# Kernel optimization log

Hardware: AMD Instinct MI355X
Metric: run time of the kernel (lower is better)

The kernel has to match this reference:

```python
import jax, jax.numpy as jnp
import numpy as np

B, T, C, H, L, V = 2, 1024, 768, 12, 6, 32000
HS = C // H  # head size 64
EPS = 1e-5


def _ln(x, g, b):
    m = jnp.mean(x, axis=-1, keepdims=True)
    v = jnp.var(x, axis=-1, keepdims=True)
    return (x - m) * jax.lax.rsqrt(v + EPS) * g + b


def setup_inputs() -> dict:
    key = jax.random.key(0)
    ks = iter(jax.random.split(key, 32))
    s = lambda *sh: jax.random.normal(next(ks), sh, jnp.float32) * 0.02
    return {
        "idx": jax.random.randint(next(ks), (B, T), 0, V),
        "tok_emb": s(V, C),
        "pos_emb": s(T, C),
        "Wq": s(L, H, C, HS), "Wk": s(L, H, C, HS), "Wv": s(L, H, C, HS),
        "Wp": s(L, C, C), "bp": jnp.zeros((L, C), jnp.float32),
        "ln1g": jnp.ones((L, C), jnp.float32), "ln1b": jnp.zeros((L, C), jnp.float32),
        "ln2g": jnp.ones((L, C), jnp.float32), "ln2b": jnp.zeros((L, C), jnp.float32),
        "W1": s(L, C, 4 * C), "b1": jnp.zeros((L, 4 * C), jnp.float32),
        "W2": s(L, 4 * C, C), "b2": jnp.zeros((L, C), jnp.float32),
        "lnfg": jnp.ones((C,), jnp.float32), "lnfb": jnp.zeros((C,), jnp.float32),
        "Wh": s(C, V), "bh": jnp.zeros((V,), jnp.float32),
    }


def reference(idx, tok_emb, pos_emb, Wq, Wk, Wv, Wp, bp, ln1g, ln1b, ln2g, ln2b,
              W1, b1, W2, b2, lnfg, lnfb, Wh, bh):
    x = tok_emb[idx] + pos_emb[None, :, :]  # [B,T,C]
    # NOTE: original scales by full embed dim C ** -0.5 (not head_size)
    scale = C ** (-0.5)
    causal = jnp.tril(jnp.ones((T, T), bool))

    def block(x, p):
        wq, wk, wv, wp, bpj, g1, be1, g2, be2, w1, bb1, w2, bb2 = p
        h = _ln(x, g1, be1)
        q = jnp.einsum('btc,hcs->bhts', h, wq)
        k = jnp.einsum('btc,hcs->bhts', h, wk)
        v = jnp.einsum('btc,hcs->bhts', h, wv)
        wei = jnp.einsum('bhts,bhus->bhtu', q, k) * scale
        wei = jnp.where(causal, wei, -jnp.inf)
        wei = jax.nn.softmax(wei, axis=-1)
        o = jnp.einsum('bhtu,bhus->bhts', wei, v)
        o = o.transpose(0, 2, 1, 3).reshape(x.shape[0], T, C)  # concat heads
        x = x + o @ wp + bpj
        h2 = _ln(x, g2, be2)
        x = x + jax.nn.relu(h2 @ w1 + bb1) @ w2 + bb2
        return x, None

    x, _ = jax.lax.scan(block, x, (Wq, Wk, Wv, Wp, bp, ln1g, ln1b, ln2g, ln2b, W1, b1, W2, b2))
    logits = _ln(x, lnfg, lnfb) @ Wh + bh  # [B,T,V]
    return logits
```

## Files before the change

kernel.cpp:

```cpp
#include <hip/hip_runtime.h>

#define B_ 2
#define T_ 1024
#define C_ 768
#define H_ 12
#define L_ 6
#define V_ 32000
#define HS_ 64
#define M_ (B_*T_)
#define C4_ (4*C_)
#define NVC_ 6400

typedef __attribute__((ext_vector_type(8))) short short8;
typedef __attribute__((ext_vector_type(4))) float f32x4;

__device__ __forceinline__ float b2f(unsigned short u) {
  union { unsigned int i; float f; } x; x.i = ((unsigned int)u) << 16; return x.f;
}
__device__ __forceinline__ unsigned short f2b(float f) {
  unsigned int u = __builtin_bit_cast(unsigned int, f);
  u += 0x7fffu + ((u >> 16) & 1u);
  return (unsigned short)(u >> 16);
}

__device__ __forceinline__ void gload16(const unsigned short* g, unsigned short* l) {
  __builtin_amdgcn_global_load_lds(
      (const __attribute__((address_space(1))) unsigned int*)g,
      (__attribute__((address_space(3))) unsigned int*)l, 16, 0, 0);
}

__global__ __launch_bounds__(256) void transpose_f2b(const float* __restrict__ in,
                                                     unsigned short* __restrict__ out,
                                                     int ldi, int ldo, size_t zi, size_t zo) {
  __shared__ unsigned short tile[32][33];
  in  += zi * blockIdx.z;
  out += zo * blockIdx.z;
  int c0 = blockIdx.x * 32, r0 = blockIdx.y * 32;
  int tx = threadIdx.x & 31, ty = threadIdx.x >> 5;
  #pragma unroll
  for (int j = 0; j < 32; j += 8)
    tile[ty + j][tx] = f2b(in[(size_t)(r0 + ty + j) * ldi + c0 + tx]);
  __syncthreads();
  #pragma unroll
  for (int j = 0; j < 32; j += 8)
    out[(size_t)(c0 + ty + j) * ldo + r0 + tx] = tile[tx][ty + j];
}

__global__ __launch_bounds__(256) void transpose_qkvp(const float* __restrict__ Wq,
                                                      const float* __restrict__ Wk,
                                                      const float* __restrict__ Wv,
                                                      const float* __restrict__ Wp,
                                                      unsigned short* __restrict__ out) {
  __shared__ unsigned short tile[32][33];
  int z = blockIdx.z;
  const float* in; unsigned short* o; int ldi; int cbase;
  if (z < 36) {
    int which = z / H_, hh = z % H_;
    in = (which == 0 ? Wq : which == 1 ? Wk : Wv) + (size_t)hh * C_ * HS_;
    o = out + (size_t)which * C_ * C_ + (size_t)hh * HS_ * C_;
    ldi = HS_; cbase = 0;
  } else {
    int ch = z - 36;
    in = Wp; ldi = C_; cbase = ch * 64;
    o = out + (size_t)3 * C_ * C_ + (size_t)ch * 64 * C_;
  }
  int c0 = blockIdx.x * 32, r0 = blockIdx.y * 32;
  int tx = threadIdx.x & 31, ty = threadIdx.x >> 5;
  #pragma unroll
  for (int j = 0; j < 32; j += 8)
    tile[ty + j][tx] = f2b(in[(size_t)(r0 + ty + j) * ldi + cbase + c0 + tx]);
  __syncthreads();
  #pragma unroll
  for (int j = 0; j < 32; j += 8)
    o[(size_t)(c0 + ty + j) * C_ + r0 + tx] = tile[tx][ty + j];
}

__global__ __launch_bounds__(256) void embed_kernel(const int* __restrict__ idx,
                                                    const float* __restrict__ tok,
                                                    const float* __restrict__ pos,
                                                    float* __restrict__ x) {
  int m = blockIdx.x;
  int t = m & (T_ - 1);
  int tk = idx[m];
  #pragma unroll
  for (int i = 0; i < 3; ++i) {
    int c = threadIdx.x + i * 256;
    x[(size_t)m * C_ + c] = tok[(size_t)tk * C_ + c] + pos[(size_t)t * C_ + c];
  }
}

__global__ __launch_bounds__(256) void ln_kernel(const float* __restrict__ x,
                                                 const float* __restrict__ g,
                                                 const float* __restrict__ bta,
                                                 unsigned short* __restrict__ h) {
  int m = blockIdx.x;
  const float* xr = x + (size_t)m * C_;
  float v[3], s = 0.f, ss = 0.f;
  #pragma unroll
  for (int i = 0; i < 3; ++i) {
    v[i] = xr[threadIdx.x + i * 256];
    s += v[i]; ss += v[i] * v[i];
  }
  #pragma unroll
  for (int off = 32; off; off >>= 1) { s += __shfl_xor(s, off); ss += __shfl_xor(ss, off); }
  __shared__ float red[8];
  int wave = threadIdx.x >> 6, lane = threadIdx.x & 63;
  if (lane == 0) { red[wave] = s; red[4 + wave] = ss; }
  __syncthreads();
  s  = red[0] + red[1] + red[2] + red[3];
  ss = red[4] + red[5] + red[6] + red[7];
  float mean = s * (1.f / C_);
  float var  = fmaxf(ss * (1.f / C_) - mean * mean, 0.f);
  float rstd = rsqrtf(var + 1e-5f);
  #pragma unroll
  for (int i = 0; i < 3; ++i) {
    int c = threadIdx.x + i * 256;
    h[(size_t)m * C_ + c] = f2b((v[i] - mean) * rstd * g[c] + bta[c]);
  }
}

__global__ __launch_bounds__(256) void attn_mfma(const unsigned short* __restrict__ q,
                                                 const unsigned short* __restrict__ k,
                                                 const unsigned short* __restrict__ v,
                                                 unsigned short* __restrict__ o) {
  const float scale = 0.03608439182435161f;
  __shared__ __align__(16) unsigned short Ks[64 * 72];
  __shared__ __align__(16) unsigned short Vt[64 * 72];
  __shared__ __align__(16) unsigned short Ps[4][16 * 72];

  int tid = threadIdx.x;
  int lane = tid & 63, wave = tid >> 6;
  int rl = lane & 15, kgrp = lane >> 4, koff = kgrp * 8;
  int qt = blockIdx.x;
  int bh = blockIdx.y;
  int hh = bh % H_, bb = bh / H_;
  size_t base = (size_t)bb * T_ * C_ + (size_t)hh * HS_;

  short8 qf0 = *(const short8*)&q[base + (size_t)(qt * 64 + wave * 16 + rl) * C_ + koff];
  short8 qf1 = *(const short8*)&q[base + (size_t)(qt * 64 + wave * 16 + rl) * C_ + 32 + koff];

  float m_[4], l_[4];
  f32x4 oacc[4];
  #pragma unroll
  for (int r = 0; r < 4; ++r) { m_[r] = -INFINITY; l_[r] = 0.f; }
  #pragma unroll
  for (int j = 0; j < 4; ++j) oacc[j] = (f32x4){0.f, 0.f, 0.f, 0.f};

  short8 kreg[2], vreg[2];
  #pragma unroll
  for (int i = 0; i < 2; ++i) {
    int e = tid + i * 256;
    kreg[i] = *(const short8*)&k[base + (size_t)(e >> 3) * C_ + (e & 7) * 8];
    vreg[i] = *(const short8*)&v[base + (size_t)(e >> 3) * C_ + (e & 7) * 8];
  }

  for (int kt = 0; kt <= qt; ++kt) {
    #pragma unroll
    for (int i = 0; i < 2; ++i) {
      int e = tid + i * 256, row = e >> 3, c8 = e & 7;
      *(short8*)&Ks[row * 72 + c8 * 8] = kreg[i];
    }
    #pragma unroll
    for (int i = 0; i < 2; ++i) {
      int e = tid + i * 256, kk = e >> 3, d8 = (e & 7) * 8;
      short8 vv = vreg[i];
      #pragma unroll
      for (int t2 = 0; t2 < 8; ++t2) {
        int ii = (t2 + tid) & 7;
        Vt[(d8 + ii) * 72 + kk] = vv[ii];
      }
    }
    __syncthreads();

    if (kt < qt) {
      #pragma unroll
      for (int i = 0; i < 2; ++i) {
        int e = tid + i * 256;
        kreg[i] = *(const short8*)&k[base + (size_t)((kt + 1) * 64 + (e >> 3)) * C_ + (e & 7) * 8];
        vreg[i] = *(const short8*)&v[base + (size_t)((kt + 1) * 64 + (e >> 3)) * C_ + (e & 7) * 8];
      }
    }

    f32x4 s[4];
    #pragma unroll
    for (int j = 0; j < 4; ++j) s[j] = (f32x4){0.f, 0.f, 0.f, 0.f};
    __builtin_amdgcn_s_setprio(1);
    #pragma unroll
    for (int j = 0; j < 4; ++j) {
      short8 b0 = *(const short8*)&Ks[(j * 16 + rl) * 72 + koff];
      short8 b1 = *(const short8*)&Ks[(j * 16 + rl) * 72 + 32 + koff];
      s[j] = __builtin_amdgcn_mfma_f32_16x16x32_bf16(qf0, b0, s[j], 0, 0, 0);
      s[j] = __builtin_amdgcn_mfma_f32_16x16x32_bf16(qf1, b1, s[j], 0, 0, 0);
    }
    __builtin_amdgcn_s_setprio(0);

    bool diag = (kt == qt);
    #pragma unroll
    for (int j = 0; j < 4; ++j)
      #pragma unroll
      for (int r = 0; r < 4; ++r) {
        float sv = s[j][r] * scale;
        if (diag) {
          int urow = j * 16 + rl, qrow = wave * 16 + kgrp * 4 + r;
          if (urow > qrow) sv = -INFINITY;
        }
        s[j][r] = sv;
      }

    float corr[4], rs[4];
    #pragma unroll
    for (int r = 0; r < 4; ++r) {
      float mrow = fmaxf(fmaxf(s[0][r], s[1][r]), fmaxf(s[2][r], s[3][r]));
      #pragma unroll
      for (int off = 8; off; off >>= 1) mrow = fmaxf(mrow, __shfl_xor(mrow, off));
      float mnew = fmaxf(m_[r], mrow);
      corr[r] = __expf(m_[r] - mnew);
      m_[r] = mnew;
    }
    #pragma unroll
    for (int r = 0; r < 4; ++r) rs[r] = 0.f;
    #pragma unroll
    for (int j = 0; j < 4; ++j)
      #pragma unroll
      for (int r = 0; r < 4; ++r) {
        float p = (s[j][r] == -INFINITY) ? 0.f : __expf(s[j][r] - m_[r]);
        s[j][r] = p;
        rs[r] += p;
      }
    #pragma unroll
    for (int r = 0; r < 4; ++r) {
      #pragma unroll
      for (int off = 8; off; off >>= 1) rs[r] += __shfl_xor(rs[r], off);
      l_[r] = l_[r] * corr[r] + rs[r];
    }
    #pragma unroll
    for (int j = 0; j < 4; ++j)
      #pragma unroll
      for (int r = 0; r < 4; ++r) oacc[j][r] *= corr[r];

    #pragma unroll
    for (int j = 0; j < 4; ++j)
      #pragma unroll
      for (int r = 0; r < 4; ++r)
        Ps[wave][(kgrp * 4 + r) * 72 + j * 16 + rl] = f2b(s[j][r]);

    short8 pa0 = *(const short8*)&Ps[wave][rl * 72 + koff];
    short8 pa1 = *(const short8*)&Ps[wave][rl * 72 + 32 + koff];
    __builtin_amdgcn_s_setprio(1);
    #pragma unroll
    for (int j = 0; j < 4; ++j) {
      short8 b0 = *(const short8*)&Vt[(j * 16 + rl) * 72 + koff];
      short8 b1 = *(const short8*)&Vt[(j * 16 + rl) * 72 + 32 + koff];
      oacc[j] = __builtin_amdgcn_mfma_f32_16x16x32_bf16(pa0, b0, oacc[j], 0, 0, 0);
      oacc[j] = __builtin_amdgcn_mfma_f32_16x16x32_bf16(pa1, b1, oacc[j], 0, 0, 0);
    }
    __builtin_amdgcn_s_setprio(0);
    __syncthreads();
  }

  #pragma unroll
  for (int j = 0; j < 4; ++j)
    #pragma unroll
    for (int r = 0; r < 4; ++r) {
      int qrow = wave * 16 + kgrp * 4 + r;
      o[base + (size_t)(qt * 64 + qrow) * C_ + j * 16 + rl] = f2b(oacc[j][r] / l_[r]);
    }
}

template<int BM, int BN, int EPI, bool MFAST>
__global__ __launch_bounds__(256) void gemm_bt(const unsigned short* __restrict__ A,
                                               const unsigned short* __restrict__ Bt,
                                               const float* __restrict__ bias,
                                               unsigned short* __restrict__ outb,
                                               float* __restrict__ outf,
                                               int M, int N, int K, int ldO,
                                               size_t zBt, size_t zOut) {
  constexpr int BK = 32;
  __shared__ __align__(16) unsigned short As[BM * BK];
  __shared__ __align__(16) unsigned short Bs[BN * BK];
  constexpr int FM = BM / 32, FN = BN / 32;

  int tid = threadIdx.x;
  int lane = tid & 63, wave = tid >> 6;
  int wr = wave >> 1, wc = wave & 1;
  int m0 = (MFAST ? blockIdx.x : blockIdx.y) * BM;
  int n0 = (MFAST ? blockIdx.y : blockIdx.x) * BN;
  int rl = lane & 15, koff = (lane >> 4) * 8;
  Bt += zBt * blockIdx.z;

  int srow = lane >> 2, sseg = (lane & 3) * 8;

  f32x4 acc[FM][FN] = {};

  for (int k0 = 0; k0 < K; k0 += BK) {
    #pragma unroll
    for (int i = 0; i < BM / 64; ++i) {
      int r = i * 64 + wave * 16;
      gload16(&A[(size_t)(m0 + r + srow) * K + k0 + sseg], &As[r * BK]);
    }
    #pragma unroll
    for (int i = 0; i < BN / 64; ++i) {
      int r = i * 64 + wave * 16;
      gload16(&Bt[(size_t)(n0 + r + srow) * K + k0 + sseg], &Bs[r * BK]);
    }
    __syncthreads();

    short8 af[FM], bfr[FN];
    #pragma unroll
    for (int i = 0; i < FM; ++i)
      af[i] = *(const short8*)&As[(wr * (BM / 2) + i * 16 + rl) * BK + koff];
    #pragma unroll
    for (int j = 0; j < FN; ++j)
      bfr[j] = *(const short8*)&Bs[(wc * (BN / 2) + j * 16 + rl) * BK + koff];
    #pragma unroll
    for (int i = 0; i < FM; ++i)
      #pragma unroll
      for (int j = 0; j < FN; ++j)
        acc[i][j] = __builtin_amdgcn_mfma_f32_16x16x32_bf16(af[i], bfr[j], acc[i][j], 0, 0, 0);
    __syncthreads();
  }

  int rbase = (lane >> 4) * 4;
  #pragma unroll
  for (int i = 0; i < FM; ++i) {
    #pragma unroll
    for (int j = 0; j < FN; ++j) {
      #pragma unroll
      for (int r = 0; r < 4; ++r) {
        int m = m0 + wr * (BM / 2) + i * 16 + rbase + r;
        int n = n0 + wc * (BN / 2) + j * 16 + (lane & 15);
        float val = acc[i][j][r];
        if (bias) val += bias[n];
        if (EPI == 0)      (outb + zOut * blockIdx.z)[(size_t)m * ldO + n] = f2b(val);
        else if (EPI == 1) (outb + zOut * blockIdx.z)[(size_t)m * ldO + n] = f2b(fmaxf(val, 0.f));
        else if (EPI == 2) (outf + zOut * blockIdx.z)[(size_t)m * ldO + n] += val;
        else               (outf + zOut * blockIdx.z)[(size_t)m * ldO + n] = val;
      }
    }
  }
}

extern "C" void kernel_launch(void* const* d_in, const int* in_sizes, int n_in,
                              void* d_out, int out_size, void* d_ws, size_t ws_size,
                              hipStream_t stream) {
  const int*   idx  = (const int*)d_in[0];
  const float* tok  = (const float*)d_in[1];
  const float* pos  = (const float*)d_in[2];
  const float* Wq   = (const float*)d_in[3];
  const float* Wk   = (const float*)d_in[4];
  const float* Wv   = (const float*)d_in[5];
  const float* Wp   = (const float*)d_in[6];
  const float* bp   = (const float*)d_in[7];
  const float* ln1g = (const float*)d_in[8];
  const float* ln1b = (const float*)d_in[9];
  const float* ln2g = (const float*)d_in[10];
  const float* ln2b = (const float*)d_in[11];
  const float* W1   = (const float*)d_in[12];
  const float* b1   = (const float*)d_in[13];
  const float* W2   = (const float*)d_in[14];
  const float* b2   = (const float*)d_in[15];
  const float* lnfg = (const float*)d_in[16];
  const float* lnfb = (const float*)d_in[17];
  const float* Wh   = (const float*)d_in[18];
  const float* bh   = (const float*)d_in[19];

  float* out = (float*)d_out;

  const size_t MC = (size_t)M_ * C_;
  const size_t fixed = MC*4 + MC*2 + MC*2*4;
  const size_t need_chunk = fixed + (size_t)NVC_*C_*2;
  const size_t need_full  = fixed + (size_t)V_*C_*2;
  if (ws_size < need_chunk) return;
  const bool full_head = (ws_size >= need_full);

  char* p = (char*)d_ws;
  float*          x   = (float*)p;            p += MC*4;
  unsigned short* h   = (unsigned short*)p;   p += MC*2;
  unsigned short* qb  = (unsigned short*)p;   p += MC*2;
  unsigned short* kb  = (unsigned short*)p;   p += MC*2;
  unsigned short* vb  = (unsigned short*)p;   p += MC*2;
  unsigned short* ob  = (unsigned short*)p;   p += MC*2;
  unsigned short* WT  = (unsigned short*)p;
  unsigned short* mid = qb;

  unsigned short* WqT = WT;
  unsigned short* WpT = WT + (size_t)3*C_*C_;
  unsigned short* W12T = WT;

  embed_kernel<<<M_, 256, 0, stream>>>(idx, tok, pos, x);

  for (int l = 0; l < L_; ++l) {
    size_t wo  = (size_t)l * C_ * C_;
    size_t wo4 = (size_t)l * C_ * C4_;
    size_t woq = (size_t)l * H_ * C_ * HS_;

    transpose_qkvp<<<dim3(HS_/32, C_/32, 48), 256, 0, stream>>>(Wq + woq, Wk + woq, Wv + woq, Wp + wo, WqT);

    ln_kernel<<<M_, 256, 0, stream>>>(x, ln1g + (size_t)l*C_, ln1b + (size_t)l*C_, h);
    gemm_bt<64,64,0,false><<<dim3(C_/64, M_/64, 3), 256, 0, stream>>>(h, WqT, nullptr, qb, nullptr,
                                                                      M_, C_, C_, C_, (size_t)C_*C_, MC);
    attn_mfma<<<dim3(T_/64, B_*H_), 256, 0, stream>>>(qb, kb, vb, ob);
    gemm_bt<64,64,2,false><<<dim3(C_/64, M_/64), 256, 0, stream>>>(ob, WpT, bp + (size_t)l*C_, nullptr, x,
                                                                   M_, C_, C_, C_, 0, 0);

    ln_kernel<<<M_, 256, 0, stream>>>(x, ln2g + (size_t)l*C_, ln2b + (size_t)l*C_, h);
    transpose_f2b<<<dim3(C4_/32, C_/32, 1), 256, 0, stream>>>(W1 + wo4, W12T, C4_, C_, 0, 0);
    gemm_bt<128,128,1,true><<<dim3(M_/128, C4_/128), 256, 0, stream>>>(h, W12T, b1 + (size_t)l*C4_, mid, nullptr,
                                                                       M_, C4_, C_, C4_, 0, 0);
    transpose_f2b<<<dim3(C_/32, C4_/32, 1), 256, 0, stream>>>(W2 + wo4, W12T, C_, C4_, 0, 0);
    gemm_bt<64,64,2,true><<<dim3(M_/64, C_/64), 256, 0, stream>>>(mid, W12T, b2 + (size_t)l*C_, nullptr, x,
                                                                  M_, C_, C4_, C_, 0, 0);
  }

  ln_kernel<<<M_, 256, 0, stream>>>(x, lnfg, lnfb, h);
  if (full_head) {
    transpose_f2b<<<dim3(V_/32, C_/32, 1), 256, 0, stream>>>(Wh, WT, V_, C_, 0, 0);
    gemm_bt<128,128,3,true><<<dim3(M_/128, V_/128), 256, 0, stream>>>(
        h, WT, bh, nullptr, out, M_, V_, C_, V_, 0, 0);
  } else {
    for (int ci = 0; ci < V_/NVC_; ++ci) {
      transpose_f2b<<<dim3(NVC_/32, C_/32, 1), 256, 0, stream>>>(Wh + (size_t)ci*NVC_, WT, V_, C_, 0, 0);
      gemm_bt<128,128,3,true><<<dim3(M_/128, NVC_/128), 256, 0, stream>>>(
          h, WT, bh + (size_t)ci*NVC_, nullptr, out + (size_t)ci*NVC_, M_, NVC_, C_, V_, 0, 0);
    }
  }
}
```

Before: 1.362 ms.

## Pair causal attention tiles per block and swizzle GEMM tiles across XCDs

The attention kernel now launches 8 blocks per head, and each block handles query tile i and then tile 15-i, so every block does the same amount of causal work and the tail imbalance goes away. Several GEMMs switch to a 1D grid, with the workgroup id remapped so that consecutive tiles land on the same XCD (the grid's id&7 round-robin), which should improve L2 reuse of shared A and B tiles. In exchange, attention gets half as many blocks (192), which may leave some CUs idle and reduces the parallelism available to hide latency.

```diff
diff --git a/kernel.cpp b/kernel.cpp
--- a/kernel.cpp
+++ b/kernel.cpp
@@ -131,150 +131,153 @@
   int tid = threadIdx.x;
   int lane = tid & 63, wave = tid >> 6;
   int rl = lane & 15, kgrp = lane >> 4, koff = kgrp * 8;
-  int qt = blockIdx.x;
   int bh = blockIdx.y;
   int hh = bh % H_, bb = bh / H_;
   size_t base = (size_t)bb * T_ * C_ + (size_t)hh * HS_;
 
-  short8 qf0 = *(const short8*)&q[base + (size_t)(qt * 64 + wave * 16 + rl) * C_ + koff];
-  short8 qf1 = *(const short8*)&q[base + (size_t)(qt * 64 + wave * 16 + rl) * C_ + 32 + koff];
-
-  float m_[4], l_[4];
-  f32x4 oacc[4];
-  #pragma unroll
-  for (int r = 0; r < 4; ++r) { m_[r] = -INFINITY; l_[r] = 0.f; }
-  #pragma unroll
-  for (int j = 0; j < 4; ++j) oacc[j] = (f32x4){0.f, 0.f, 0.f, 0.f};
-
-  short8 kreg[2], vreg[2];
-  #pragma unroll
-  for (int i = 0; i < 2; ++i) {
-    int e = tid + i * 256;
-    kreg[i] = *(const short8*)&k[base + (size_t)(e >> 3) * C_ + (e & 7) * 8];
-    vreg[i] = *(const short8*)&v[base + (size_t)(e >> 3) * C_ + (e & 7) * 8];
-  }
-
-  for (int kt = 0; kt <= qt; ++kt) {
+  for (int pass = 0; pass < 2; ++pass) {
+    int qt = pass ? (15 - (int)blockIdx.x) : (int)blockIdx.x;
+
+    short8 qf0 = *(const short8*)&q[base + (size_t)(qt * 64 + wave * 16 + rl) * C_ + koff];
+    short8 qf1 = *(const short8*)&q[base + (size_t)(qt * 64 + wave * 16 + rl) * C_ + 32 + koff];
+
+    float m_[4], l_[4];
+    f32x4 oacc[4];
+    #pragma unroll
+    for (int r = 0; r < 4; ++r) { m_[r] = -INFINITY; l_[r] = 0.f; }
+    #pragma unroll
+    for (int j = 0; j < 4; ++j) oacc[j] = (f32x4){0.f, 0.f, 0.f, 0.f};
+
+    short8 kreg[2], vreg[2];
     #pragma unroll
     for (int i = 0; i < 2; ++i) {
-      int e = tid + i * 256, row = e >> 3, c8 = e & 7;
-      *(short8*)&Ks[row * 72 + c8 * 8] = kreg[i];
-    }
-    #pragma unroll
-    for (int i = 0; i < 2; ++i) {
-      int e = tid + i * 256, kk = e >> 3, d8 = (e & 7) * 8;
-      short8 vv = vreg[i];
-      #pragma unroll
-      for (int t2 = 0; t2 < 8; ++t2) {
-        int ii = (t2 + tid) & 7;
-        Vt[(d8 + ii) * 72 + kk] = vv[ii];
-      }
-    }
-    __syncthreads();
-
-    if (kt < qt) {
+      int e = tid + i * 256;
+      kreg[i] = *(const short8*)&k[base + (size_t)(e >> 3) * C_ + (e & 7) * 8];
+      vreg[i] = *(const short8*)&v[base + (size_t)(e >> 3) * C_ + (e & 7) * 8];
+    }
+
+    for (int kt = 0; kt <= qt; ++kt) {
       #pragma unroll
       for (int i = 0; i < 2; ++i) {
-        int e = tid + i * 256;
-        kreg[i] = *(const short8*)&k[base + (size_t)((kt + 1) * 64 + (e >> 3)) * C_ + (e & 7) * 8];
-        vreg[i] = *(const short8*)&v[base + (size_t)((kt + 1) * 64 + (e >> 3)) * C_ + (e & 7) * 8];
-      }
-    }
-
-    f32x4 s[4];
-    #pragma unroll
-    for (int j = 0; j < 4; ++j) s[j] = (f32x4){0.f, 0.f, 0.f, 0.f};
-    __builtin_amdgcn_s_setprio(1);
-    #pragma unroll
-    for (int j = 0; j < 4; ++j) {
-      short8 b0 = *(const short8*)&Ks[(j * 16 + rl) * 72 + koff];
-      short8 b1 = *(const short8*)&Ks[(j * 16 + rl) * 72 + 32 + koff];
-      s[j] = __builtin_amdgcn_mfma_f32_16x16x32_bf16(qf0, b0, s[j], 0, 0, 0);
-      s[j] = __builtin_amdgcn_mfma_f32_16x16x32_bf16(qf1, b1, s[j], 0, 0, 0);
-    }
-    __builtin_amdgcn_s_setprio(0);
-
-    bool diag = (kt == qt);
+        int e = tid + i * 256, row = e >> 3, c8 = e & 7;
+        *(short8*)&Ks[row * 72 + c8 * 8] = kreg[i];
+      }
+      #pragma unroll
+      for (int i = 0; i < 2; ++i) {
+        int e = tid + i * 256, kk = e >> 3, d8 = (e & 7) * 8;
+        short8 vv = vreg[i];
+        #pragma unroll
+        for (int t2 = 0; t2 < 8; ++t2) {
+          int ii = (t2 + tid) & 7;
+          Vt[(d8 + ii) * 72 + kk] = vv[ii];
+        }
+      }
+      __syncthreads();
+
+      if (kt < qt) {
+        #pragma unroll
+        for (int i = 0; i < 2; ++i) {
+          int e = tid + i * 256;
+          kreg[i] = *(const short8*)&k[base + (size_t)((kt + 1) * 64 + (e >> 3)) * C_ + (e & 7) * 8];
+          vreg[i] = *(const short8*)&v[base + (size_t)((kt + 1) * 64 + (e >> 3)) * C_ + (e & 7) * 8];
+        }
+      }
+
+      f32x4 s[4];
+      #pragma unroll
+      for (int j = 0; j < 4; ++j) s[j] = (f32x4){0.f, 0.f, 0.f, 0.f};
+      __builtin_amdgcn_s_setprio(1);
+      #pragma unroll
+      for (int j = 0; j < 4; ++j) {
+        short8 b0 = *(const short8*)&Ks[(j * 16 + rl) * 72 + koff];
+        short8 b1 = *(const short8*)&Ks[(j * 16 + rl) * 72 + 32 + koff];
+        s[j] = __builtin_amdgcn_mfma_f32_16x16x32_bf16(qf0, b0, s[j], 0, 0, 0);
+        s[j] = __builtin_amdgcn_mfma_f32_16x16x32_bf16(qf1, b1, s[j], 0, 0, 0);
+      }
+      __builtin_amdgcn_s_setprio(0);
+
+      bool diag = (kt == qt);
+      #pragma unroll
+      for (int j = 0; j < 4; ++j)
+        #pragma unroll
+        for (int r = 0; r < 4; ++r) {
+          float sv = s[j][r] * scale;
+          if (diag) {
+            int urow = j * 16 + rl, qrow = wave * 16 + kgrp * 4 + r;
+            if (urow > qrow) sv = -INFINITY;
+          }
+          s[j][r] = sv;
+        }
+
+      float corr[4], rs[4];
+      #pragma unroll
+      for (int r = 0; r < 4; ++r) {
+        float mrow = fmaxf(fmaxf(s[0][r], s[1][r]), fmaxf(s[2][r], s[3][r]));
+        #pragma unroll
+        for (int off = 8; off; off >>= 1) mrow = fmaxf(mrow, __shfl_xor(mrow, off));
+        float mnew = fmaxf(m_[r], mrow);
+        corr[r] = __expf(m_[r] - mnew);
+        m_[r] = mnew;
+      }
+      #pragma unroll
+      for (int r = 0; r < 4; ++r) rs[r] = 0.f;
+      #pragma unroll
+      for (int j = 0; j < 4; ++j)
+        #pragma unroll
+        for (int r = 0; r < 4; ++r) {
+          float p = (s[j][r] == -INFINITY) ? 0.f : __expf(s[j][r] - m_[r]);
+          s[j][r] = p;
+          rs[r] += p;
+        }
+      #pragma unroll
+      for (int r = 0; r < 4; ++r) {
+        #pragma unroll
+        for (int off = 8; off; off >>= 1) rs[r] += __shfl_xor(rs[r], off);
+        l_[r] = l_[r] * corr[r] + rs[r];
+      }
+      #pragma unroll
+      for (int j = 0; j < 4; ++j)
+        #pragma unroll
+        for (int r = 0; r < 4; ++r) oacc[j][r] *= corr[r];
+
+      #pragma unroll
+      for (int j = 0; j < 4; ++j)
+        #pragma unroll
+        for (int r = 0; r < 4; ++r)
+          Ps[wave][(kgrp * 4 + r) * 72 + j * 16 + rl] = f2b(s[j][r]);
+
+      short8 pa0 = *(const short8*)&Ps[wave][rl * 72 + koff];
+      short8 pa1 = *(const short8*)&Ps[wave][rl * 72 + 32 + koff];
+      __builtin_amdgcn_s_setprio(1);
+      #pragma unroll
+      for (int j = 0; j < 4; ++j) {
+        short8 b0 = *(const short8*)&Vt[(j * 16 + rl) * 72 + koff];
+        short8 b1 = *(const short8*)&Vt[(j * 16 + rl) * 72 + 32 + koff];
+        oacc[j] = __builtin_amdgcn_mfma_f32_16x16x32_bf16(pa0, b0, oacc[j], 0, 0, 0);
+        oacc[j] = __builtin_amdgcn_mfma_f32_16x16x32_bf16(pa1, b1, oacc[j], 0, 0, 0);
+      }
+      __builtin_amdgcn_s_setprio(0);
+      __syncthreads();
+    }
+
     #pragma unroll
     for (int j = 0; j < 4; ++j)
       #pragma unroll
       for (int r = 0; r < 4; ++r) {
-        float sv = s[j][r] * scale;
-        if (diag) {
-          int urow = j * 16 + rl, qrow = wave * 16 + kgrp * 4 + r;
-          if (urow > qrow) sv = -INFINITY;
-        }
-        s[j][r] = sv;
-      }
-
-    float corr[4], rs[4];
-    #pragma unroll
-    for (int r = 0; r < 4; ++r) {
-      float mrow = fmaxf(fmaxf(s[0][r], s[1][r]), fmaxf(s[2][r], s[3][r]));
-      #pragma unroll
-      for (int off = 8; off; off >>= 1) mrow = fmaxf(mrow, __shfl_xor(mrow, off));
-      float mnew = fmaxf(m_[r], mrow);
-      corr[r] = __expf(m_[r] - mnew);
-      m_[r] = mnew;
-    }
-    #pragma unroll
-    for (int r = 0; r < 4; ++r) rs[r] = 0.f;
-    #pragma unroll
-    for (int j = 0; j < 4; ++j)
-      #pragma unroll
-      for (int r = 0; r < 4; ++r) {
-        float p = (s[j][r] == -INFINITY) ? 0.f : __expf(s[j][r] - m_[r]);
-        s[j][r] = p;
-        rs[r] += p;
-      }
-    #pragma unroll
-    for (int r = 0; r < 4; ++r) {
-      #pragma unroll
-      for (int off = 8; off; off >>= 1) rs[r] += __shfl_xor(rs[r], off);
-      l_[r] = l_[r] * corr[r] + rs[r];
-    }
-    #pragma unroll
-    for (int j = 0; j < 4; ++j)
-      #pragma unroll
-      for (int r = 0; r < 4; ++r) oacc[j][r] *= corr[r];
-
-    #pragma unroll
-    for (int j = 0; j < 4; ++j)
-      #pragma unroll
-      for (int r = 0; r < 4; ++r)
-        Ps[wave][(kgrp * 4 + r) * 72 + j * 16 + rl] = f2b(s[j][r]);
-
-    short8 pa0 = *(const short8*)&Ps[wave][rl * 72 + koff];
-    short8 pa1 = *(const short8*)&Ps[wave][rl * 72 + 32 + koff];
-    __builtin_amdgcn_s_setprio(1);
-    #pragma unroll
-    for (int j = 0; j < 4; ++j) {
-      short8 b0 = *(const short8*)&Vt[(j * 16 + rl) * 72 + koff];
-      short8 b1 = *(const short8*)&Vt[(j * 16 + rl) * 72 + 32 + koff];
-      oacc[j] = __builtin_amdgcn_mfma_f32_16x16x32_bf16(pa0, b0, oacc[j], 0, 0, 0);
-      oacc[j] = __builtin_amdgcn_mfma_f32_16x16x32_bf16(pa1, b1, oacc[j], 0, 0, 0);
-    }
-    __builtin_amdgcn_s_setprio(0);
-    __syncthreads();
-  }
-
-  #pragma unroll
-  for (int j = 0; j < 4; ++j)
-    #pragma unroll
-    for (int r = 0; r < 4; ++r) {
-      int qrow = wave * 16 + kgrp * 4 + r;
-      o[base + (size_t)(qt * 64 + qrow) * C_ + j * 16 + rl] = f2b(oacc[j][r] / l_[r]);
-    }
-}
-
-template<int BM, int BN, int EPI, bool MFAST>
+        int qrow = wave * 16 + kgrp * 4 + r;
+        o[base + (size_t)(qt * 64 + qrow) * C_ + j * 16 + rl] = f2b(oacc[j][r] / l_[r]);
+      }
+  }
+}
+
+template<int BM, int BN, int EPI, bool MFAST, bool SWZ>
 __global__ __launch_bounds__(256) void gemm_bt(const unsigned short* __restrict__ A,
                                                const unsigned short* __restrict__ Bt,
                                                const float* __restrict__ bias,
                                                unsigned short* __restrict__ outb,
                                                float* __restrict__ outf,
                                                int M, int N, int K, int ldO,
-                                               size_t zBt, size_t zOut) {
+                                               size_t zBt, size_t zOut, int nMt) {
   constexpr int BK = 32;
   __shared__ __align__(16) unsigned short As[BM * BK];
   __shared__ __align__(16) unsigned short Bs[BN * BK];
@@ -283,8 +286,18 @@
   int tid = threadIdx.x;
   int lane = tid & 63, wave = tid >> 6;
   int wr = wave >> 1, wc = wave & 1;
-  int m0 = (MFAST ? blockIdx.x : blockIdx.y) * BM;
-  int n0 = (MFAST ? blockIdx.y : blockIdx.x) * BN;
+  int m0, n0;
+  if (SWZ) {
+    int nwg = gridDim.x, wg = blockIdx.x;
+    int qq = nwg >> 3, rr = nwg & 7;
+    int xcd = wg & 7, off = wg >> 3;
+    int wgid = (xcd < rr ? xcd * (qq + 1) : rr * (qq + 1) + (xcd - rr) * qq) + off;
+    m0 = (wgid % nMt) * BM;
+    n0 = (wgid / nMt) * BN;
+  } else {
+    m0 = (MFAST ? blockIdx.x : blockIdx.y) * BM;
+    n0 = (MFAST ? blockIdx.y : blockIdx.x) * BN;
+  }
   int rl = lane & 15, koff = (lane >> 4) * 8;
   Bt += zBt * blockIdx.z;
 
@@ -397,31 +410,31 @@
     transpose_qkvp<<<dim3(HS_/32, C_/32, 48), 256, 0, stream>>>(Wq + woq, Wk + woq, Wv + woq, Wp + wo, WqT);
 
     ln_kernel<<<M_, 256, 0, stream>>>(x, ln1g + (size_t)l*C_, ln1b + (size_t)l*C_, h);
-    gemm_bt<64,64,0,false><<<dim3(C_/64, M_/64, 3), 256, 0, stream>>>(h, WqT, nullptr, qb, nullptr,
-                                                                      M_, C_, C_, C_, (size_t)C_*C_, MC);
-    attn_mfma<<<dim3(T_/64, B_*H_), 256, 0, stream>>>(qb, kb, vb, ob);
-    gemm_bt<64,64,2,false><<<dim3(C_/64, M_/64), 256, 0, stream>>>(ob, WpT, bp + (size_t)l*C_, nullptr, x,
-                                                                   M_, C_, C_, C_, 0, 0);
+    gemm_bt<64,64,0,false,false><<<dim3(C_/64, M_/64, 3), 256, 0, stream>>>(h, WqT, nullptr, qb, nullptr,
+                                                                            M_, C_, C_, C_, (size_t)C_*C_, MC, 0);
+    attn_mfma<<<dim3(8, B_*H_), 256, 0, stream>>>(qb, kb, vb, ob);
+    gemm_bt<64,64,2,false,false><<<dim3(C_/64, M_/64), 256, 0, stream>>>(ob, WpT, bp + (size_t)l*C_, nullptr, x,
+                                                                         M_, C_, C_, C_, 0, 0, 0);
 
     ln_kernel<<<M_, 256, 0, stream>>>(x, ln2g + (size_t)l*C_, ln2b + (size_t)l*C_, h);
     transpose_f2b<<<dim3(C4_/32, C_/32, 1), 256, 0, stream>>>(W1 + wo4, W12T, C4_, C_, 0, 0);
-    gemm_bt<128,128,1,true><<<dim3(M_/128, C4_/128), 256, 0, stream>>>(h, W12T, b1 + (size_t)l*C4_, mid, nullptr,
-                                                                       M_, C4_, C_, C4_, 0, 0);
+    gemm_bt<128,128,1,true,true><<<dim3((M_/128)*(C4_/128)), 256, 0, stream>>>(h, W12T, b1 + (size_t)l*C4_, mid, nullptr,
+                                                                               M_, C4_, C_, C4_, 0, 0, M_/128);
     transpose_f2b<<<dim3(C_/32, C4_/32, 1), 256, 0, stream>>>(W2 + wo4, W12T, C_, C4_, 0, 0);
-    gemm_bt<64,64,2,true><<<dim3(M_/64, C_/64), 256, 0, stream>>>(mid, W12T, b2 + (size_t)l*C_, nullptr, x,
-                                                                  M_, C_, C4_, C_, 0, 0);
+    gemm_bt<64,64,2,true,true><<<dim3((M_/64)*(C_/64)), 256, 0, stream>>>(mid, W12T, b2 + (size_t)l*C_, nullptr, x,
+                                                                          M_, C_, C4_, C_, 0, 0, M_/64);
   }
 
   ln_kernel<<<M_, 256, 0, stream>>>(x, lnfg, lnfb, h);
   if (full_head) {
     transpose_f2b<<<dim3(V_/32, C_/32, 1), 256, 0, stream>>>(Wh, WT, V_, C_, 0, 0);
-    gemm_bt<128,128,3,true><<<dim3(M_/128, V_/128), 256, 0, stream>>>(
-        h, WT, bh, nullptr, out, M_, V_, C_, V_, 0, 0);
+    gemm_bt<128,128,3,true,true><<<dim3((M_/128)*(V_/128)), 256, 0, stream>>>(
+        h, WT, bh, nullptr, out, M_, V_, C_, V_, 0, 0, M_/128);
   } else {
     for (int ci = 0; ci < V_/NVC_; ++ci) {
       transpose_f2b<<<dim3(NVC_/32, C_/32, 1), 256, 0, stream>>>(Wh + (size_t)ci*NVC_, WT, V_, C_, 0, 0);
-      gemm_bt<128,128,3,true><<<dim3(M_/128, NVC_/128), 256, 0, stream>>>(
-          h, WT, bh + (size_t)ci*NVC_, nullptr, out + (size_t)ci*NVC_, M_, NVC_, C_, V_, 0, 0);
-    }
-  }
-}
+      gemm_bt<128,128,3,true,true><<<dim3((M_/128)*(NVC_/128)), 256, 0, stream>>>(
+          h, WT, bh + (size_t)ci*NVC_, nullptr, out + (size_t)ci*NVC_, M_, NVC_, C_, V_, 0, 0, M_/128);
+    }
+  }
+}
```

Result: faster. 1.310 ms (-3.8%).
